# Kernel optimization log

Hardware: AMD Instinct MI355X
Metric: run time of the kernel (lower is better)

Reference implementation:

```python
import jax, jax.numpy as jnp
import numpy as np

SIZES = (1, 2, 4, 8)
C_IN = 64
KC = C_IN // 8      # key_channels = out_channels // 8 = 8
VC = C_IN           # value_channels = out_channels = 64
N_STAGES = len(SIZES)


def setup_inputs() -> dict:
    key = jax.random.key(0)
    ks = jax.random.split(key, 16)
    N, C, H, W = 1, C_IN, 64, 64
    inp = {
        "x1": jax.random.normal(ks[0], (N, C, H, W), jnp.float32),
        "x2": jax.random.normal(ks[1], (N, C, H, W), jnp.float32),
        # per-stage 1x1 conv weights (stacked over the 4 PAM stages)
        "Wq": jax.random.normal(ks[2], (N_STAGES, KC, C), jnp.float32) * 0.02,
        "bq": jnp.zeros((N_STAGES, KC), jnp.float32),
        "gammaq": 1.0 + jax.random.normal(ks[3], (N_STAGES, KC), jnp.float32) * 0.02,
        "betaq": jnp.zeros((N_STAGES, KC), jnp.float32),
        "Wk": jax.random.normal(ks[4], (N_STAGES, KC, C), jnp.float32) * 0.02,
        "bk": jnp.zeros((N_STAGES, KC), jnp.float32),
        "gammak": 1.0 + jax.random.normal(ks[5], (N_STAGES, KC), jnp.float32) * 0.02,
        "betak": jnp.zeros((N_STAGES, KC), jnp.float32),
        "Wv": jax.random.normal(ks[6], (N_STAGES, VC, C), jnp.float32) * 0.02,
        "bv": jnp.zeros((N_STAGES, VC), jnp.float32),
        # final 1x1 conv: in = C * n_stages, out = C, no bias
        "Wo": jax.random.normal(ks[7], (C, VC * N_STAGES), jnp.float32) * 0.02,
    }
    return inp


def _pam_block(x, Wq, bq, gq, betq, Wk, bk, gk, betk, Wv, bv, scale):
    # x: [N, C, H, 2W] (two images concatenated along width)
    N, C, H, W2 = x.shape
    w = W2 // 2
    kc = Wq.shape[0]

    def proj(W, b):  # 1x1 conv
        return jnp.einsum('nchw,kc->nkhw', x, W) + b[:, None, None]

    # BatchNorm (inference form: zero running mean / unit variance) folded to affine
    q = gq[:, None, None] * proj(Wq, bq) + betq[:, None, None]
    k = gk[:, None, None] * proj(Wk, bk) + betk[:, None, None]
    v = proj(Wv, bv)

    hl, wl = H // scale, w // scale

    def to_blocks(t):
        ch = t.shape[1]
        # stack left/right halves on a trailing axis: [N, ch, H, w, 2]
        t = jnp.stack([t[..., :w], t[..., w:]], axis=-1)
        # split into scale x scale spatial blocks -> [N, s*s, ch, hl*wl*2]
        t = t.reshape(N, ch, scale, hl, scale, wl, 2)
        t = t.transpose(0, 2, 4, 1, 3, 5, 6)
        return t.reshape(N, scale * scale, ch, hl * wl * 2)

    qb, kb, vb = to_blocks(q), to_blocks(k), to_blocks(v)

    sim = jnp.einsum('nbkp,nbkq->nbpq', qb, kb) * (kc ** -0.5)
    att = jax.nn.softmax(sim, axis=-1)
    # context = V @ att^T : ctx[c,p] = sum_q v[c,q] * att[p,q]
    ctx = jnp.einsum('nbcq,nbpq->nbcp', vb, att)

    Cv = Wv.shape[0]
    ctx = ctx.reshape(N, scale, scale, Cv, hl, wl, 2)
    ctx = ctx.transpose(0, 3, 1, 4, 2, 5, 6).reshape(N, Cv, H, w, 2)
    # re-concatenate the two halves along width -> [N, Cv, H, 2w]
    return jnp.concatenate([ctx[..., 0], ctx[..., 1]], axis=3)


def reference(x1, x2, Wq, bq, gammaq, betaq, Wk, bk, gammak, betak, Wv, bv, Wo):
    h_w = x1.shape[3]
    x = jnp.concatenate([x1, x2], axis=3)  # [N, C, H, 2W]
    priors = [
        _pam_block(x, Wq[i], bq[i], gammaq[i], betaq[i],
                   Wk[i], bk[i], gammak[i], betak[i],
                   Wv[i], bv[i], SIZES[i])
        for i in range(N_STAGES)
    ]
    cat = jnp.concatenate(priors, axis=1)  # [N, 4C, H, 2W]
    out = jnp.einsum('ndhw,od->nohw', cat, Wo)  # final 1x1 conv, no bias
    return out[:, :, :, :h_w], out[:, :, :, h_w:]


if __name__ == '__main__':
    o1, o2 = reference(**setup_inputs())
    print(o1.shape, o2.shape)
```

## Files before the change

kernel.cpp:

```cpp
#include <hip/hip_runtime.h>


typedef short bf16x8 __attribute__((ext_vector_type(8)));
typedef float f32x16 __attribute__((ext_vector_type(16)));

__device__ __forceinline__ float bf2f(unsigned short u){ union{unsigned int i;float f;}v; v.i=((unsigned int)u)<<16; return v.f; }
__device__ __forceinline__ unsigned short f2bf(float f){
    union{float f;unsigned int i;}v; v.f=f;
    unsigned int r = v.i + 0x7fffu + ((v.i>>16)&1u);
    return (unsigned short)(r>>16);
}
__device__ __forceinline__ float exp2fast(float x){ return __builtin_amdgcn_exp2f(x); }

#define QMUL 0.5100697233f

__global__ __launch_bounds__(256) void proj_all_kernel(
    const float* __restrict__ x1, const float* __restrict__ x2,
    const float* __restrict__ Wq, const float* __restrict__ bq,
    const float* __restrict__ gq, const float* __restrict__ beq,
    const float* __restrict__ Wk, const float* __restrict__ bk,
    const float* __restrict__ gk, const float* __restrict__ bek,
    const float* __restrict__ Wv, const float* __restrict__ bv,
    unsigned short* __restrict__ Qb, unsigned short* __restrict__ Kb,
    unsigned short* __restrict__ Vf)
{
    __shared__ __align__(16) float xs[64][68];
    __shared__ __align__(16) unsigned int vqk[64][8];
    __shared__ __align__(16) unsigned short vv[64][64];

    const int wg = blockIdx.x, st = wg >> 7, chunk = wg & 127;
    const int lgP = 13 - 2*st, Pm1 = (1<<lgP) - 1;
    const int hb = 6 - st, wlm = (1<<hb) - 1;
    const int t = threadIdx.x;
    const int gp0 = chunk*64;
    const int blk = gp0 >> lgP, p0 = gp0 & Pm1;
    const int si = blk >> st, sj = blk & ((1<<st)-1);
    const int hwbase = ((si<<hb)<<6) | (sj<<hb);

    for (int idx = t; idx < 4096; idx += 256) {
        int c = idx >> 6, g = idx & 63;
        int p = p0 + g, half = p & 1, pw = p >> 1;
        int hw = hwbase | ((pw>>hb)<<6) | (pw & wlm);
        xs[g][c] = (half ? x2 : x1)[c*4096 + hw];
    }
    __syncthreads();

    const int px = t & 63, wv = t >> 6;
    float xr[64];
    #pragma unroll
    for (int q4 = 0; q4 < 16; ++q4)
        *(float4*)&xr[q4*4] = *(const float4*)&xs[px][q4*4];

#define VRANGE(LO,HI)                                              \
    for (int ch = (LO); ch < (HI); ++ch) {                         \
        const float* wp = Wv + (st*64 + ch)*64;                    \
        float d = bv[st*64 + ch];                                  \
        _Pragma("unroll")                                          \
        for (int k = 0; k < 64; ++k) d += wp[k]*xr[k];             \
        vv[ch][px] = f2bf(d);                                      \
    }

    if (wv == 0) {
        unsigned short qo[8], ko[8];
        for (int ch = 0; ch < 8; ++ch) {
            const float* wp = Wq + (st*8 + ch)*64;
            float d = 0.f;
            #pragma unroll
            for (int k = 0; k < 64; ++k) d += wp[k]*xr[k];
            float gm = gq[st*8+ch];
            qo[ch] = f2bf((gm*(d + bq[st*8+ch]) + beq[st*8+ch])*QMUL);
        }
        for (int ch = 0; ch < 8; ++ch) {
            const float* wp = Wk + (st*8 + ch)*64;
            float d = 0.f;
            #pragma unroll
            for (int k = 0; k < 64; ++k) d += wp[k]*xr[k];
            float gm = gk[st*8+ch];
            ko[ch] = f2bf(gm*(d + bk[st*8+ch]) + bek[st*8+ch]);
        }
        #pragma unroll
        for (int i = 0; i < 4; ++i) {
            vqk[px][i]   = (unsigned)qo[2*i] | ((unsigned)qo[2*i+1] << 16);
            vqk[px][4+i] = (unsigned)ko[2*i] | ((unsigned)ko[2*i+1] << 16);
        }
        VRANGE(0, 4)
    } else if (wv == 1) { VRANGE(4, 24) }
    else if   (wv == 2) { VRANGE(24, 44) }
    else                { VRANGE(44, 64) }
#undef VRANGE
    __syncthreads();

    if (t < 64) {
        *(uint4*)(Qb + st*65536 + (gp0 + t)*8) = *(const uint4*)&vqk[t][0];
    } else if (t < 128) {
        int p2 = t - 64;
        *(uint4*)(Kb + st*65536 + (gp0 + p2)*8) = *(const uint4*)&vqk[p2][4];
    }
    unsigned short* Vst = Vf + st*524288 + (blk << (lgP+6));
    #pragma unroll
    for (int r = 0; r < 2; ++r) {
        int task = t + r*256;
        int ch = task >> 3, o = task & 7;
        *(uint4*)(Vst + (ch << lgP) + p0 + o*8) = *(const uint4*)&vv[ch][o*8];
    }
}

__global__ __launch_bounds__(256) void attn_kernel(
    const unsigned short* __restrict__ Qb, const unsigned short* __restrict__ Kb,
    const unsigned short* __restrict__ Vf,
    float* __restrict__ PART, float* __restrict__ LPART)
{
    __shared__ __align__(16) unsigned short Ps[4][2304];

    const int wg = blockIdx.x;
    const int t = threadIdx.x, lane = t & 63, wv = t >> 6;
    const int l31 = lane & 31, lhi = lane >> 5;

    int st, qt, slot, kbase, nkw;
    if (wg < 512)       { st=0; qt=wg>>1;  slot=wg&1;
                          kbase=(wg&1)*4096 + wv*1024; nkw=1024; }
    else if (wg < 1024) { int r=wg-512;  st=1; qt=r>>1; slot=2+(r&1);
                          kbase=(r&1)*1024 + wv*256;  nkw=256; }
    else if (wg < 1280) { st=2; qt=wg-1024; slot=4; kbase=wv*128; nkw=128; }
    else                { st=3; qt=wg-1280; slot=5; kbase=wv*64;
                          nkw=(wv<2)?64:0; }

    const int lgP = 13 - 2*st, P = 1 << lgP;
    const int blk = qt >> (lgP - 5);
    const int q0  = (qt & ((P>>5)-1)) * 32;

    const unsigned short* Qg = Qb + st*65536 + blk*P*8;
    const unsigned short* Kg = Kb + st*65536 + blk*P*8;
    const unsigned short* Vg = Vf + st*524288 + blk*P*64;

    bf16x8 qa;
    #pragma unroll
    for (int j = 0; j < 8; ++j) qa[j] = 0;
    if (lane < 32) qa = *(const bf16x8*)(Qg + (q0 + l31)*8);

    f32x16 acc0, acc1;
    #pragma unroll
    for (int r = 0; r < 16; ++r) { acc0[r] = 0.f; acc1[r] = 0.f; }
    float lsum_reg = 0.f;

    unsigned short* Pw = Ps[wv];
    for (int k0 = kbase; k0 < kbase + nkw; k0 += 64) {
        bf16x8 kb0 = *(const bf16x8*)(Kg + (k0 + l31)*8);
        bf16x8 kb1 = *(const bf16x8*)(Kg + (k0 + 32 + l31)*8);
        f32x16 S0, S1;
        #pragma unroll
        for (int r = 0; r < 16; ++r) { S0[r] = 0.f; S1[r] = 0.f; }
        S0 = __builtin_amdgcn_mfma_f32_32x32x16_bf16(qa, kb0, S0, 0, 0, 0);
        S1 = __builtin_amdgcn_mfma_f32_32x32x16_bf16(qa, kb1, S1, 0, 0, 0);

        #pragma unroll
        for (int r = 0; r < 16; ++r) {
            int qrow = (r&3) + 8*(r>>2) + 4*lhi;
            Pw[qrow*72 + l31]      = f2bf(exp2fast(S0[r]));
            Pw[qrow*72 + 32 + l31] = f2bf(exp2fast(S1[r]));
        }

        float lpart = 0.f;
        bf16x8 pa[4];
        #pragma unroll
        for (int kc = 0; kc < 4; ++kc) {
            pa[kc] = *(const bf16x8*)(Pw + l31*72 + kc*16 + 8*lhi);
            #pragma unroll
            for (int j = 0; j < 8; ++j)
                lpart += bf2f((unsigned short)pa[kc][j]);
        }
        lpart += __shfl_xor(lpart, 32, 64);
        lsum_reg += lpart;

        #pragma unroll
        for (int kc = 0; kc < 4; ++kc) {
            const int ko = k0 + kc*16 + 8*lhi;
            bf16x8 vb0 = *(const bf16x8*)(Vg + l31*P + ko);
            bf16x8 vb1 = *(const bf16x8*)(Vg + (32 + l31)*P + ko);
            acc0 = __builtin_amdgcn_mfma_f32_32x32x16_bf16(pa[kc], vb0, acc0, 0, 0, 0);
            acc1 = __builtin_amdgcn_mfma_f32_32x32x16_bf16(pa[kc], vb1, acc1, 0, 0, 0);
        }
    }

    float* B0 = (float*)&Ps[0][0];
    float* B1 = B0 + 2048;
    float* Lm = B0 + 4096;
    __syncthreads();
    if (wv == 0 || wv == 2) {
        float* B = (wv == 0) ? B0 : B1;
        #pragma unroll
        for (int r = 0; r < 16; ++r) {
            int qrow = (r&3) + 8*(r>>2) + 4*lhi;
            B[qrow*64 + l31]      = acc0[r];
            B[qrow*64 + 32 + l31] = acc1[r];
        }
        if (lane < 32) Lm[(wv>>1)*32 + l31] = lsum_reg;
    }
    __syncthreads();
    if (wv == 1 || wv == 3) {
        float* B = (wv == 1) ? B0 : B1;
        #pragma unroll
        for (int r = 0; r < 16; ++r) {
            int qrow = (r&3) + 8*(r>>2) + 4*lhi;
            B[qrow*64 + l31]      += acc0[r];
            B[qrow*64 + 32 + l31] += acc1[r];
        }
        if (lane < 32) Lm[(wv>>1)*32 + l31] += lsum_reg;
    }
    __syncthreads();

    float4* Pslab4 = (float4*)(PART + slot*524288 + qt*2048);
    const float4* B04 = (const float4*)B0;
    const float4* B14 = (const float4*)B1;
    #pragma unroll
    for (int r = 0; r < 2; ++r) {
        int idx = t + r*256;
        float4 a = B04[idx], b = B14[idx];
        Pslab4[idx] = float4{a.x+b.x, a.y+b.y, a.z+b.z, a.w+b.w};
    }
    if (t < 32)
        LPART[slot*8192 + qt*32 + t] = Lm[t] + Lm[32 + t];
}

__global__ __launch_bounds__(256) void normconv_kernel(
    const float* __restrict__ PART, const float* __restrict__ LPART,
    const float* __restrict__ Wo, float* __restrict__ out)
{
    __shared__ __align__(16) unsigned short csb[32][264];
    __shared__ __align__(16) unsigned short wof[16384];
    __shared__ float voutf[64][33];
    __shared__ float linv[4][32];
    __shared__ int gpar[4][32];
    const int t = threadIdx.x;
    const int px0 = blockIdx.x * 32;

    {
        int oc = t >> 2, d0 = (t & 3) * 64;
        for (int b = 0; b < 8; ++b) {
            int d = d0 + b*8;
            float4 w0 = *(const float4*)(Wo + oc*256 + d);
            float4 w1 = *(const float4*)(Wo + oc*256 + d + 4);
            unsigned short tmp[8];
            tmp[0]=f2bf(w0.x); tmp[1]=f2bf(w0.y); tmp[2]=f2bf(w0.z); tmp[3]=f2bf(w0.w);
            tmp[4]=f2bf(w1.x); tmp[5]=f2bf(w1.y); tmp[6]=f2bf(w1.z); tmp[7]=f2bf(w1.w);
            *(uint4*)&wof[(d>>3)*512 + oc*8] = *(const uint4*)tmp;
        }
    }
    if (t < 128) {
        const int s0tab[4] = {0,2,4,5};
        const int sctab[4] = {2,2,1,1};
        int stt = t >> 5, i = t & 31;
        int pix = px0 + i;
        int half = pix >> 12, hw = pix & 4095;
        int h = hw >> 6, w = hw & 63;
        int hb = 6 - stt, wlm = (1<<hb)-1;
        int si = h >> hb, sj = w >> hb, hi = h & wlm, wi = w & wlm;
        int blk = (si << stt) | sj;
        int p = (((hi << hb) | wi) << 1) | half;
        int gp = blk*(8192>>(2*stt)) + p;
        gpar[stt][i] = gp;
        int s0 = s0tab[stt];
        float l = LPART[s0*8192 + gp];
        if (sctab[stt] == 2) l += LPART[(s0+1)*8192 + gp];
        linv[stt][i] = 1.f / l;
    }
    __syncthreads();

    {
        const int s0tab[4] = {0,2,4,5};
        int gpx = t >> 3, cvg = (t & 7) * 8;
        for (int stt = 0; stt < 4; ++stt) {
            int gp = gpar[stt][gpx];
            const float* p = PART + s0tab[stt]*524288
                           + (gp>>5)*2048 + (gp&31)*64 + cvg;
            float4 a = *(const float4*)p;
            float4 b = *(const float4*)(p + 4);
            if (stt < 2) {
                float4 a2 = *(const float4*)(p + 524288);
                float4 b2 = *(const float4*)(p + 524288 + 4);
                a.x+=a2.x; a.y+=a2.y; a.z+=a2.z; a.w+=a2.w;
                b.x+=b2.x; b.y+=b2.y; b.z+=b2.z; b.w+=b2.w;
            }
            float li = linv[stt][gpx];
            unsigned short tmp[8];
            tmp[0]=f2bf(a.x*li); tmp[1]=f2bf(a.y*li); tmp[2]=f2bf(a.z*li); tmp[3]=f2bf(a.w*li);
            tmp[4]=f2bf(b.x*li); tmp[5]=f2bf(b.y*li); tmp[6]=f2bf(b.z*li); tmp[7]=f2bf(b.w*li);
            *(uint4*)&csb[gpx][stt*64 + cvg] = *(const uint4*)tmp;
        }
    }
    __syncthreads();

    const int lane = t & 63, wvv = t >> 6;
    const int l31 = lane & 31, lhi = lane >> 5;
    const int nh = wvv & 1, kh = wvv >> 1;
    f32x16 acc;
    #pragma unroll
    for (int r = 0; r < 16; ++r) acc[r] = 0.f;
    #pragma unroll
    for (int s = 0; s < 8; ++s) {
        int dg = kh*16 + s*2 + lhi;
        bf16x8 a = *(const bf16x8*)&csb[l31][kh*128 + s*16 + 8*lhi];
        bf16x8 b = *(const bf16x8*)&wof[dg*512 + (nh*32 + l31)*8];
        acc = __builtin_amdgcn_mfma_f32_32x32x16_bf16(a, b, acc, 0, 0, 0);
    }
    if (kh == 0) {
        #pragma unroll
        for (int r = 0; r < 16; ++r)
            voutf[nh*32 + l31][(r&3) + 8*(r>>2) + 4*lhi] = acc[r];
    }
    __syncthreads();
    if (kh == 1) {
        #pragma unroll
        for (int r = 0; r < 16; ++r)
            voutf[nh*32 + l31][(r&3) + 8*(r>>2) + 4*lhi] += acc[r];
    }
    __syncthreads();

    const int half = px0 >> 12, hw0 = px0 & 4095;
    float* obase = out + half*262144 + hw0;
    #pragma unroll
    for (int r = 0; r < 8; ++r) {
        int idx = t + r*256;
        int oc = idx >> 5, pxi = idx & 31;
        obase[oc*4096 + pxi] = voutf[oc][pxi];
    }
}

extern "C" void kernel_launch(void* const* d_in, const int* in_sizes, int n_in,
                              void* d_out, int out_size, void* d_ws, size_t ws_size,
                              hipStream_t stream)
{
    (void)out_size; (void)ws_size;
    const float *x1, *x2, *Wq, *bq, *gq, *beq, *Wk, *bk, *gk, *bek, *Wv, *bv, *Wo;

    if (n_in >= 13 && in_sizes[0] == 2048) {
        Wk  = (const float*)d_in[0];  Wo  = (const float*)d_in[1];
        Wq  = (const float*)d_in[2];  Wv  = (const float*)d_in[3];
        bek = (const float*)d_in[4];  beq = (const float*)d_in[5];
        bk  = (const float*)d_in[6];  bq  = (const float*)d_in[7];
        bv  = (const float*)d_in[8];  gk  = (const float*)d_in[9];
        gq  = (const float*)d_in[10];
        x1  = (const float*)d_in[11]; x2  = (const float*)d_in[12];
    } else {
        x1  = (const float*)d_in[0];  x2  = (const float*)d_in[1];
        Wq  = (const float*)d_in[2];  bq  = (const float*)d_in[3];
        gq  = (const float*)d_in[4];  beq = (const float*)d_in[5];
        Wk  = (const float*)d_in[6];  bk  = (const float*)d_in[7];
        gk  = (const float*)d_in[8];  bek = (const float*)d_in[9];
        Wv  = (const float*)d_in[10]; bv  = (const float*)d_in[11];
        Wo  = (const float*)d_in[12];
    }

    unsigned short* Qb = (unsigned short*)d_ws;
    unsigned short* Kb = Qb + 262144;
    unsigned short* Vf = Kb + 262144;
    float* PART  = (float*)d_ws + 1310720;
    float* LPART = PART + 3145728;

    proj_all_kernel<<<512, 256, 0, stream>>>(x1,x2,Wq,bq,gq,beq,Wk,bk,gk,bek,Wv,bv,Qb,Kb,Vf);
    attn_kernel<<<1536, 256, 0, stream>>>(Qb,Kb,Vf,PART,LPART);
    normconv_kernel<<<256, 256, 0, stream>>>(PART, LPART, Wo, (float*)d_out);
}
```

Baseline: 165.1 us.

## Switch Q/K/V/P to fp16, split projection across two workgroups, sum rows in registers

The projection kernel now runs twice as many workgroups, with each pair of workgroups splitting the 64 V channels and the Q/K work, which raises parallelism in that stage. Q, K, V and P are stored as fp16 using packed round-toward-zero conversion, and the attention uses fp16 MFMA instead of bf16. Softmax row sums are accumulated in registers from the fp32 exponentials rather than re-read from LDS and converted every tile. V is written in an interleaved pixel order with the P LDS row stride changed, and the reduction happens once after the loop. fp16 narrows the range for exp values, which risks overflow if scores grow large, and each pixel chunk's x tile is now loaded twice.

```diff
diff --git a/kernel.cpp b/kernel.cpp
--- a/kernel.cpp
+++ b/kernel.cpp
@@ -1,14 +1,20 @@
 #include <hip/hip_runtime.h>
 
 
-typedef short bf16x8 __attribute__((ext_vector_type(8)));
+typedef _Float16 f16x8 __attribute__((ext_vector_type(8)));
 typedef float f32x16 __attribute__((ext_vector_type(16)));
 
-__device__ __forceinline__ float bf2f(unsigned short u){ union{unsigned int i;float f;}v; v.i=((unsigned int)u)<<16; return v.f; }
 __device__ __forceinline__ unsigned short f2bf(float f){
     union{float f;unsigned int i;}v; v.f=f;
     unsigned int r = v.i + 0x7fffu + ((v.i>>16)&1u);
     return (unsigned short)(r>>16);
+}
+__device__ __forceinline__ unsigned short f2h(float f){
+    union{_Float16 h; unsigned short u;}v; v.h = (_Float16)f; return v.u;
+}
+__device__ __forceinline__ unsigned pack2h(float a, float b){
+    auto pk = __builtin_amdgcn_cvt_pkrtz(a, b);
+    unsigned u; __builtin_memcpy(&u, &pk, 4); return u;
 }
 __device__ __forceinline__ float exp2fast(float x){ return __builtin_amdgcn_exp2f(x); }
 
@@ -25,10 +31,11 @@
     unsigned short* __restrict__ Vf)
 {
     __shared__ __align__(16) float xs[64][68];
-    __shared__ __align__(16) unsigned int vqk[64][8];
+    __shared__ __align__(16) unsigned vqk[64][8];
     __shared__ __align__(16) unsigned short vv[64][64];
 
-    const int wg = blockIdx.x, st = wg >> 7, chunk = wg & 127;
+    const int wg = blockIdx.x, st = wg >> 8, rr = wg & 255;
+    const int chunk = rr >> 1, cgrp = rr & 1;
     const int lgP = 13 - 2*st, Pm1 = (1<<lgP) - 1;
     const int hb = 6 - st, wlm = (1<<hb) - 1;
     const int t = threadIdx.x;
@@ -57,51 +64,78 @@
         float d = bv[st*64 + ch];                                  \
         _Pragma("unroll")                                          \
         for (int k = 0; k < 64; ++k) d += wp[k]*xr[k];             \
-        vv[ch][px] = f2bf(d);                                      \
-    }
-
-    if (wv == 0) {
-        unsigned short qo[8], ko[8];
-        for (int ch = 0; ch < 8; ++ch) {
-            const float* wp = Wq + (st*8 + ch)*64;
-            float d = 0.f;
+        vv[ch][px] = f2h(d);                                       \
+    }
+#define KPROJ(CH,DST)                                              \
+    {   const float* wp = Wk + (st*8 + (CH))*64;                   \
+        float d = 0.f;                                             \
+        _Pragma("unroll")                                          \
+        for (int k = 0; k < 64; ++k) d += wp[k]*xr[k];             \
+        float gm = gk[st*8+(CH)];                                  \
+        (DST) = gm*(d + bk[st*8+(CH)]) + bek[st*8+(CH)]; }
+
+    if (cgrp == 0) {
+        if (wv == 0) {
+            float qv8[8];
+            for (int ch = 0; ch < 8; ++ch) {
+                const float* wp = Wq + (st*8 + ch)*64;
+                float d = 0.f;
+                #pragma unroll
+                for (int k = 0; k < 64; ++k) d += wp[k]*xr[k];
+                float gm = gq[st*8+ch];
+                qv8[ch] = (gm*(d + bq[st*8+ch]) + beq[st*8+ch])*QMUL;
+            }
             #pragma unroll
-            for (int k = 0; k < 64; ++k) d += wp[k]*xr[k];
-            float gm = gq[st*8+ch];
-            qo[ch] = f2bf((gm*(d + bq[st*8+ch]) + beq[st*8+ch])*QMUL);
-        }
-        for (int ch = 0; ch < 8; ++ch) {
-            const float* wp = Wk + (st*8 + ch)*64;
-            float d = 0.f;
+            for (int i = 0; i < 4; ++i) vqk[px][i] = pack2h(qv8[2*i], qv8[2*i+1]);
+            float k0v, k1v; KPROJ(0, k0v) KPROJ(1, k1v)
+            vqk[px][4] = pack2h(k0v, k1v);
+        } else if (wv == 1) {
+            float ka, kb2;
+            KPROJ(2, ka) KPROJ(3, kb2) vqk[px][5] = pack2h(ka, kb2);
+            KPROJ(4, ka) KPROJ(5, kb2) vqk[px][6] = pack2h(ka, kb2);
+            KPROJ(6, ka) KPROJ(7, kb2) vqk[px][7] = pack2h(ka, kb2);
+            VRANGE(0, 4)
+        } else if (wv == 2) { VRANGE(4, 14) }
+        else               { VRANGE(14, 24) }
+    } else {
+        if      (wv == 0) { VRANGE(24, 34) }
+        else if (wv == 1) { VRANGE(34, 44) }
+        else if (wv == 2) { VRANGE(44, 54) }
+        else              { VRANGE(54, 64) }
+    }
+#undef VRANGE
+#undef KPROJ
+    __syncthreads();
+
+    unsigned short* Vst = Vf + st*524288 + (blk << (lgP+6));
+    if (cgrp == 0) {
+        if (t < 64) {
+            *(uint4*)(Qb + st*65536 + (gp0 + t)*8) = *(const uint4*)&vqk[t][0];
+        } else if (t < 128) {
+            int p2 = t - 64;
+            *(uint4*)(Kb + st*65536 + (gp0 + p2)*8) = *(const uint4*)&vqk[p2][4];
+        }
+        if (t < 192) {
+            int ch = t >> 3, o = t & 7;
+            unsigned short tmp[8];
             #pragma unroll
-            for (int k = 0; k < 64; ++k) d += wp[k]*xr[k];
-            float gm = gk[st*8+ch];
-            ko[ch] = f2bf(gm*(d + bk[st*8+ch]) + bek[st*8+ch]);
-        }
-        #pragma unroll
-        for (int i = 0; i < 4; ++i) {
-            vqk[px][i]   = (unsigned)qo[2*i] | ((unsigned)qo[2*i+1] << 16);
-            vqk[px][4+i] = (unsigned)ko[2*i] | ((unsigned)ko[2*i+1] << 16);
-        }
-        VRANGE(0, 4)
-    } else if (wv == 1) { VRANGE(4, 24) }
-    else if   (wv == 2) { VRANGE(24, 44) }
-    else                { VRANGE(44, 64) }
-#undef VRANGE
-    __syncthreads();
-
-    if (t < 64) {
-        *(uint4*)(Qb + st*65536 + (gp0 + t)*8) = *(const uint4*)&vqk[t][0];
-    } else if (t < 128) {
-        int p2 = t - 64;
-        *(uint4*)(Kb + st*65536 + (gp0 + p2)*8) = *(const uint4*)&vqk[p2][4];
-    }
-    unsigned short* Vst = Vf + st*524288 + (blk << (lgP+6));
-    #pragma unroll
-    for (int r = 0; r < 2; ++r) {
-        int task = t + r*256;
-        int ch = task >> 3, o = task & 7;
-        *(uint4*)(Vst + (ch << lgP) + p0 + o*8) = *(const uint4*)&vv[ch][o*8];
+            for (int u = 0; u < 8; ++u) {
+                int s = o*8 + u;
+                tmp[u] = vv[ch][((s&1)<<5) | (s>>1)];
+            }
+            *(uint4*)(Vst + (ch << lgP) + p0 + o*8) = *(const uint4*)tmp;
+        }
+    } else {
+        for (int task = t; task < 320; task += 256) {
+            int ch = 24 + (task >> 3), o = task & 7;
+            unsigned short tmp[8];
+            #pragma unroll
+            for (int u = 0; u < 8; ++u) {
+                int s = o*8 + u;
+                tmp[u] = vv[ch][((s&1)<<5) | (s>>1)];
+            }
+            *(uint4*)(Vst + (ch << lgP) + p0 + o*8) = *(const uint4*)tmp;
+        }
     }
 }
 
@@ -110,7 +144,7 @@
     const unsigned short* __restrict__ Vf,
     float* __restrict__ PART, float* __restrict__ LPART)
 {
-    __shared__ __align__(16) unsigned short Ps[4][2304];
+    __shared__ __align__(16) unsigned short Ps[4][2432];
 
     const int wg = blockIdx.x;
     const int t = threadIdx.x, lane = t & 63, wv = t >> 6;
@@ -133,53 +167,59 @@
     const unsigned short* Kg = Kb + st*65536 + blk*P*8;
     const unsigned short* Vg = Vf + st*524288 + blk*P*64;
 
-    bf16x8 qa;
-    #pragma unroll
-    for (int j = 0; j < 8; ++j) qa[j] = 0;
-    if (lane < 32) qa = *(const bf16x8*)(Qg + (q0 + l31)*8);
+    f16x8 qa;
+    #pragma unroll
+    for (int j = 0; j < 8; ++j) qa[j] = (_Float16)0.f;
+    if (lane < 32) qa = *(const f16x8*)(Qg + (q0 + l31)*8);
 
     f32x16 acc0, acc1;
     #pragma unroll
     for (int r = 0; r < 16; ++r) { acc0[r] = 0.f; acc1[r] = 0.f; }
+    float rowsum[16];
+    #pragma unroll
+    for (int r = 0; r < 16; ++r) rowsum[r] = 0.f;
+
+    unsigned short* Pw = Ps[wv];
+    unsigned* Pw32 = (unsigned*)Pw;
+    for (int k0 = kbase; k0 < kbase + nkw; k0 += 64) {
+        f16x8 kb0 = *(const f16x8*)(Kg + (k0 + l31)*8);
+        f16x8 kb1 = *(const f16x8*)(Kg + (k0 + 32 + l31)*8);
+        f32x16 S0, S1;
+        #pragma unroll
+        for (int r = 0; r < 16; ++r) { S0[r] = 0.f; S1[r] = 0.f; }
+        S0 = __builtin_amdgcn_mfma_f32_32x32x16_f16(qa, kb0, S0, 0, 0, 0);
+        S1 = __builtin_amdgcn_mfma_f32_32x32x16_f16(qa, kb1, S1, 0, 0, 0);
+
+        #pragma unroll
+        for (int r = 0; r < 16; ++r) {
+            float p0 = exp2fast(S0[r]);
+            float p1 = exp2fast(S1[r]);
+            rowsum[r] += p0 + p1;
+            int qrow = (r&3) + 8*(r>>2) + 4*lhi;
+            Pw32[qrow*38 + l31] = pack2h(p0, p1);
+        }
+
+        #pragma unroll
+        for (int kc = 0; kc < 4; ++kc) {
+            f16x8 pa  = *(const f16x8*)(Pw + l31*76 + kc*16 + 8*lhi);
+            const int ko = k0 + kc*16 + 8*lhi;
+            f16x8 vb0 = *(const f16x8*)(Vg + l31*P + ko);
+            f16x8 vb1 = *(const f16x8*)(Vg + (32 + l31)*P + ko);
+            acc0 = __builtin_amdgcn_mfma_f32_32x32x16_f16(pa, vb0, acc0, 0, 0, 0);
+            acc1 = __builtin_amdgcn_mfma_f32_32x32x16_f16(pa, vb1, acc1, 0, 0, 0);
+        }
+    }
+
+    float* SC = (float*)Pw;
+    #pragma unroll
+    for (int r = 0; r < 16; ++r) {
+        int qrow = (r&3) + 8*(r>>2) + 4*lhi;
+        SC[qrow*33 + l31] = rowsum[r];
+    }
     float lsum_reg = 0.f;
-
-    unsigned short* Pw = Ps[wv];
-    for (int k0 = kbase; k0 < kbase + nkw; k0 += 64) {
-        bf16x8 kb0 = *(const bf16x8*)(Kg + (k0 + l31)*8);
-        bf16x8 kb1 = *(const bf16x8*)(Kg + (k0 + 32 + l31)*8);
-        f32x16 S0, S1;
-        #pragma unroll
-        for (int r = 0; r < 16; ++r) { S0[r] = 0.f; S1[r] = 0.f; }
-        S0 = __builtin_amdgcn_mfma_f32_32x32x16_bf16(qa, kb0, S0, 0, 0, 0);
-        S1 = __builtin_amdgcn_mfma_f32_32x32x16_bf16(qa, kb1, S1, 0, 0, 0);
-
-        #pragma unroll
-        for (int r = 0; r < 16; ++r) {
-            int qrow = (r&3) + 8*(r>>2) + 4*lhi;
-            Pw[qrow*72 + l31]      = f2bf(exp2fast(S0[r]));
-            Pw[qrow*72 + 32 + l31] = f2bf(exp2fast(S1[r]));
-        }
-
-        float lpart = 0.f;
-        bf16x8 pa[4];
-        #pragma unroll
-        for (int kc = 0; kc < 4; ++kc) {
-            pa[kc] = *(const bf16x8*)(Pw + l31*72 + kc*16 + 8*lhi);
-            #pragma unroll
-            for (int j = 0; j < 8; ++j)
-                lpart += bf2f((unsigned short)pa[kc][j]);
-        }
-        lpart += __shfl_xor(lpart, 32, 64);
-        lsum_reg += lpart;
-
-        #pragma unroll
-        for (int kc = 0; kc < 4; ++kc) {
-            const int ko = k0 + kc*16 + 8*lhi;
-            bf16x8 vb0 = *(const bf16x8*)(Vg + l31*P + ko);
-            bf16x8 vb1 = *(const bf16x8*)(Vg + (32 + l31)*P + ko);
-            acc0 = __builtin_amdgcn_mfma_f32_32x32x16_bf16(pa[kc], vb0, acc0, 0, 0, 0);
-            acc1 = __builtin_amdgcn_mfma_f32_32x32x16_bf16(pa[kc], vb1, acc1, 0, 0, 0);
-        }
+    if (lane < 32) {
+        #pragma unroll 8
+        for (int j = 0; j < 32; ++j) lsum_reg += SC[l31*33 + j];
     }
 
     float* B0 = (float*)&Ps[0][0];
@@ -221,6 +261,8 @@
     if (t < 32)
         LPART[slot*8192 + qt*32 + t] = Lm[t] + Lm[32 + t];
 }
+
+typedef short bf16x8 __attribute__((ext_vector_type(8)));
 
 __global__ __launch_bounds__(256) void normconv_kernel(
     const float* __restrict__ PART, const float* __restrict__ LPART,
@@ -357,7 +399,7 @@
     float* PART  = (float*)d_ws + 1310720;
     float* LPART = PART + 3145728;
 
-    proj_all_kernel<<<512, 256, 0, stream>>>(x1,x2,Wq,bq,gq,beq,Wk,bk,gk,bek,Wv,bv,Qb,Kb,Vf);
+    proj_all_kernel<<<1024, 256, 0, stream>>>(x1,x2,Wq,bq,gq,beq,Wk,bk,gk,bek,Wv,bv,Qb,Kb,Vf);
     attn_kernel<<<1536, 256, 0, stream>>>(Qb,Kb,Vf,PART,LPART);
     normconv_kernel<<<256, 256, 0, stream>>>(PART, LPART, Wo, (float*)d_out);
 }
```

Result: slower. 169.1 us (+2.4%).
